# Optimization experiments

Hardware: AMD Instinct MI355X
Metric: run time of the kernel (lower is better)

The kernel has to match this reference:

```python
import jax, jax.numpy as jnp
from jax import lax
import numpy as np

B, N_WAY, K_SHOT, Q, IMG = 8, 5, 1, 15, 84
D = 3      # repnet spatial output for imgsz=84
CF = 64    # repnet channels
C2 = CF + 2

def _conv(x, w, b):
    y = lax.conv_general_dilated(x, w, (1, 1), 'VALID', dimension_numbers=('NCHW', 'OIHW', 'NCHW'))
    return y + b[None, :, None, None]

def _maxpool2(x):
    return lax.reduce_window(x, -jnp.inf, lax.max, (1, 1, 2, 2), (1, 1, 2, 2), 'VALID')

def _avgpool5(x):
    return lax.reduce_window(x, 0.0, lax.add, (1, 1, 5, 5), (1, 1, 5, 5), 'VALID') / 25.0

def _bn(x, g, b):
    # train-mode BatchNorm2d: batch statistics over (N, H, W), biased variance, eps=1e-5
    m = jnp.mean(x, (0, 2, 3), keepdims=True)
    v = jnp.var(x, (0, 2, 3), keepdims=True)
    return (x - m) * lax.rsqrt(v + 1e-5) * g[None, :, None, None] + b[None, :, None, None]

def _repnet(x, cw1, cb1, bg1, bb1, cw2, cb2, bg2, bb2, cw3, cb3, bg3, bb3, cw4, cb4, bg4, bb4):
    x = jax.nn.relu(_bn(_maxpool2(_conv(x, cw1, cb1)), bg1, bb1))
    x = jax.nn.relu(_bn(_maxpool2(_conv(x, cw2, cb2)), bg2, bb2))
    x = jax.nn.relu(_bn(_conv(x, cw3, cb3), bg3, bb3))
    x = jax.nn.relu(_bn(_conv(x, cw4, cb4), bg4, bb4))
    return _avgpool5(x)

def _forward(support_x, support_y, query_x, query_y, cw1, cb1, bg1, bb1, cw2, cb2, bg2, bb2, cw3, cb3, bg3, bb3, cw4, cb4, bg4, bb4, gW1, gb1, gW2, gb2, gW3, gb3, gW4, gb4, fW1, fb1, fW2, fb2, fW3, fb3, fW4, fb4):
    b, setsz = support_x.shape[:2]
    q = query_x.shape[1]
    rep = lambda z: _repnet(z, cw1, cb1, bg1, bb1, cw2, cb2, bg2, bb2, cw3, cb3, bg3, bb3, cw4, cb4, bg4, bb4)
    sup = rep(support_x.reshape(b * setsz, 3, IMG, IMG)).reshape(b, setsz, CF, D, D)
    qry = rep(query_x.reshape(b * q, 3, IMG, IMG)).reshape(b, q, CF, D, D)
    sup = sup.reshape(b, N_WAY, K_SHOT, CF, D, D).sum(2)  # sum over shots -> (b, n_way, c, d, d)
    setsz = N_WAY
    sy = support_y[:, ::K_SHOT]
    ii, jj = jnp.meshgrid(jnp.arange(D), jnp.arange(D), indexing='ij')
    coord = jnp.stack([ii, jj]).astype(jnp.float32) / D  # (2, d, d): ch0 = i/d, ch1 = j/d
    sup = jnp.concatenate([sup, jnp.broadcast_to(coord, (b, setsz, 2, D, D))], axis=2)  # (b,s,66,d,d)
    qry = jnp.concatenate([qry, jnp.broadcast_to(coord, (b, q, 2, D, D))], axis=2)      # (b,q,66,d,d)
    d2 = D * D
    sup = sup.reshape(b, setsz, C2, d2)
    qry = qry.reshape(b, q, C2, d2)
    # pair feature is cat([support_feat, query_feat]); split g's first layer so the
    # (b,q,s,d2,d2,2c) pair tensor is never materialized: g1([s;q]) = s@Ws + q@Wq + b1
    Ws, Wq = gW1[:C2], gW1[C2:]
    A = jnp.einsum('bscp,ck->bspk', sup, Ws)   # (b, s, d2, 256)
    Bq = jnp.einsum('bqcp,ck->bqpk', qry, Wq)  # (b, q, d2, 256)
    h = jax.nn.relu(A[:, None, :, :, None, :] + Bq[:, :, None, None, :, :] + gb1)  # (b,q,s,d2,d2,256)
    h = jax.nn.relu(h @ gW2 + gb2)
    h = jax.nn.relu(h @ gW3 + gb3)
    h = jax.nn.relu(h @ gW4 + gb4)
    x_f = h.sum((3, 4))  # sum over all d2*d2 pixel pairs -> (b, q, s, 256)
    h = jax.nn.relu(x_f @ fW1 + fb1)
    h = jax.nn.relu(h @ fW2 + fb2)  # nn.Dropout treated as identity (deterministic reference)
    h = jax.nn.relu(h @ fW3 + fb3)
    o = h @ fW4 + fb4  # (b, q, s, 64)
    score = jnp.sqrt(jnp.sum(o * o, axis=-1))  # L2 norm over feature dim -> (b, q, s)
    n = jnp.sqrt(jnp.sum(score * score, axis=2, keepdims=True))
    score = score / n * (n * n / (1.0 + n * n))  # squash
    ap = sy[:, None, :] == query_y[:, :, None]  # exactly one True per (b, q)
    an = ~ap
    score_ap = jnp.sum(jnp.where(ap, score, 0.0), axis=2, keepdims=True)
    MARGIN = 0.2
    loss = jnp.sum(jax.nn.relu(score - score_ap + MARGIN) * an)
    return loss

def setup_inputs() -> dict:
    key = jax.random.key(0)
    ks = iter(jax.random.split(key, 48))
    nrm = lambda shape, s: jax.random.normal(next(ks), shape, jnp.float32) * s
    inp = {}
    inp['support_x'] = nrm((B, N_WAY * K_SHOT, 3, IMG, IMG), 1.0)
    inp['support_y'] = jnp.tile(jnp.arange(N_WAY, dtype=jnp.int32), (B, 1))
    inp['query_x'] = nrm((B, Q, 3, IMG, IMG), 1.0)
    inp['query_y'] = jax.random.randint(next(ks), (B, Q), 0, N_WAY, dtype=jnp.int32)
    inp['cw1'] = nrm((64, 3, 3, 3), 0.19); inp['cb1'] = nrm((64,), 0.02)
    inp['bg1'] = 1.0 + nrm((64,), 0.05); inp['bb1'] = nrm((64,), 0.02)
    inp['cw2'] = nrm((64, 64, 3, 3), 0.042); inp['cb2'] = nrm((64,), 0.02)
    inp['bg2'] = 1.0 + nrm((64,), 0.05); inp['bb2'] = nrm((64,), 0.02)
    inp['cw3'] = nrm((64, 64, 3, 3), 0.042); inp['cb3'] = nrm((64,), 0.02)
    inp['bg3'] = 1.0 + nrm((64,), 0.05); inp['bb3'] = nrm((64,), 0.02)
    inp['cw4'] = nrm((64, 64, 3, 3), 0.042); inp['cb4'] = nrm((64,), 0.02)
    inp['bg4'] = 1.0 + nrm((64,), 0.05); inp['bb4'] = nrm((64,), 0.02)
    inp['gW1'] = nrm((2 * C2, 256), 0.087); inp['gb1'] = nrm((256,), 0.02)
    inp['gW2'] = nrm((256, 256), 0.0625); inp['gb2'] = nrm((256,), 0.02)
    inp['gW3'] = nrm((256, 256), 0.0625); inp['gb3'] = nrm((256,), 0.02)
    inp['gW4'] = nrm((256, 256), 0.0625); inp['gb4'] = nrm((256,), 0.02)
    inp['fW1'] = nrm((256, 256), 0.0625); inp['fb1'] = nrm((256,), 0.02)
    inp['fW2'] = nrm((256, 256), 0.0625); inp['fb2'] = nrm((256,), 0.02)
    inp['fW3'] = nrm((256, 128), 0.0625); inp['fb3'] = nrm((128,), 0.02)
    inp['fW4'] = nrm((128, 64), 0.088); inp['fb4'] = nrm((64,), 0.02)
    return inp

def reference(support_x, support_y, query_x, query_y, cw1, cb1, bg1, bb1, cw2, cb2, bg2, bb2, cw3, cb3, bg3, bb3, cw4, cb4, bg4, bb4, gW1, gb1, gW2, gb2, gW3, gb3, gW4, gb4, fW1, fb1, fW2, fb2, fW3, fb3, fW4, fb4):
    return _forward(support_x, support_y, query_x, query_y, cw1, cb1, bg1, bb1, cw2, cb2, bg2, bb2, cw3, cb3, bg3, bb3, cw4, cb4, bg4, bb4, gW1, gb1, gW2, gb2, gW3, gb3, gW4, gb4, fW1, fb1, fW2, fb2, fW3, fb3, fW4, fb4)
```

## Files before the change

### kernel.cpp

```cpp
#include <hip/hip_runtime.h>
#include <hip/hip_bf16.h>

typedef __hip_bfloat16 bf16;
typedef __attribute__((ext_vector_type(8))) short short8;
typedef __attribute__((ext_vector_type(4))) short bfx4;
typedef __attribute__((ext_vector_type(4))) float f32x4;

#define DEV __device__ __forceinline__

static constexpr int NSUP = 40;
static constexpr int NQRY = 120;
static constexpr int NIMG = 160;
static constexpr int GM   = 48600;
static constexpr int GMP  = 48640;
static constexpr int NBS  = 128;
static constexpr int NBQ  = 384;

DEV float b2f(short s) {
    union { unsigned int u; float f; } v; v.u = ((unsigned int)(unsigned short)s) << 16; return v.f;
}
DEV short bfbits(float v) {
    bf16 h = __float2bfloat16(v);
    union { bf16 b; short s; } u; u.b = h; return u.s;
}

DEV int xcd_swz(int b, int nwg) {
    int q = nwg >> 3, r = nwg & 7;
    int x = b & 7, i = b >> 3;
    return (x < r) ? x * (q + 1) + i : r * (q + 1) + (x - r) * q + i;
}

#define GLL(gp, lp) __builtin_amdgcn_global_load_lds( \
    (const __attribute__((address_space(1))) void*)(gp), \
    (__attribute__((address_space(3))) void*)(lp), 16, 0, 0)

__global__ void nhwc4_kernel(const float* sx, const float* qx, bf16* img) {
    int idx = blockIdx.x * 256 + threadIdx.x;
    if (idx >= NIMG * 7056) return;
    int n = idx / 7056, p = idx % 7056;
    const float* im = ((n < NSUP) ? sx + (size_t)n * 3 * 7056 : qx + (size_t)(n - NSUP) * 3 * 7056) + p;
    bfx4 o;
    o[0] = bfbits(im[0]);
    o[1] = bfbits(im[7056]);
    o[2] = bfbits(im[14112]);
    o[3] = 0;
    *(bfx4*)&img[(size_t)idx * 4] = o;
}

__global__ void prep_kernel(const float* cw1, const float* cw2, const float* cw3,
                            const float* cw4, const float* gW2, const float* gW3,
                            const float* gW4, const float* fW1, const float* fW2,
                            const float* fW3, const float* fW4, const float* fb4,
                            bf16* Wc1, bf16* Wp, bf16* WTg, bf16* fWT, float* fb4p) {
    int idx = blockIdx.x * 256 + threadIdx.x;
    if (idx < 4096) {
        int oc = idx >> 6, k = idx & 63;
        int ky = k >> 4, r = k & 15;
        float v = 0.f;
        if (ky < 3 && r < 12) {
            int kx = r >> 2, ic = r & 3;
            if (ic < 3) v = cw1[oc * 27 + ic * 9 + ky * 3 + kx];
        }
        Wc1[idx] = __float2bfloat16(v);
        return;
    }
    idx -= 4096;
    if (idx < 3 * 64 * 584) {
        int L = idx / (64 * 584), r = idx % (64 * 584);
        int oc = r / 584, kk = r % 584;
        const float* src = (L == 0) ? cw2 : (L == 1) ? cw3 : cw4;
        float v = 0.f;
        if (kk < 576) {
            int ic = kk & 63, tap = kk >> 6;
            v = src[oc * 576 + ic * 9 + tap];
        }
        Wp[idx] = __float2bfloat16(v);
        return;
    }
    idx -= 3 * 64 * 584;
    if (idx < 3 * 65536) {
        int L = idx >> 16, r = idx & 65535, n = r >> 8, k = r & 255;
        const float* W = (L == 0) ? gW2 : (L == 1) ? gW3 : gW4;
        WTg[idx] = __float2bfloat16(W[k * 256 + n]);
        return;
    }
    idx -= 3 * 65536;
    if (idx < 65536) {
        int n = idx >> 8, k = idx & 255;
        fWT[idx] = __float2bfloat16(fW1[k * 256 + n]);
    } else if (idx < 131072) {
        int r = idx - 65536, n = r >> 8, k = r & 255;
        fWT[idx] = __float2bfloat16(fW2[k * 256 + n]);
    } else if (idx < 163840) {
        int r = idx - 131072, n = r >> 8, k = r & 255;
        fWT[idx] = __float2bfloat16(fW3[k * 128 + n]);
    } else if (idx < 180224) {
        int r = idx - 163840, n = r >> 7, k = r & 127;
        float v = (n < 64) ? fW4[k * 64 + n] : 0.f;
        fWT[idx] = __float2bfloat16(v);
    } else if (idx < 180352) {
        int i = idx - 180224;
        fb4p[i] = (i < 64) ? fb4[i] : 0.f;
    }
}

__global__ __launch_bounds__(256) void conv1m_kernel(
        const bf16* __restrict__ img, const bf16* __restrict__ Wc1,
        const float* __restrict__ cb1, bf16* __restrict__ out) {
    int wid = xcd_swz(blockIdx.x, NIMG * 27);
    int n = wid / 27, chunk = wid % 27;
    int wv = threadIdx.x >> 6, ln = threadIdx.x & 63;
    int pr = ln & 15, kg = ln >> 4;
    int t0 = (chunk * 4 + wv) * 16;
    int t = t0 + pr;
    int tc = t < 1681 ? t : 1680;
    int pyt = tc / 41, pxt = tc % 41;
    const bf16* ib = img + (size_t)n * 28224;

    short8 wf[4][2];
    #pragma unroll
    for (int mt = 0; mt < 4; ++mt)
        #pragma unroll
        for (int h = 0; h < 2; ++h)
            wf[mt][h] = *(const short8*)&Wc1[(size_t)(mt * 16 + pr) * 64 + h * 32 + kg * 8];

    int r8 = (kg & 1) * 8;
    int kyb = kg >> 1;
    short8 pf[4][2];
    #pragma unroll
    for (int nt = 0; nt < 4; ++nt) {
        int py = 2 * pyt + (nt >> 1), px = 2 * pxt + (nt & 1);
        #pragma unroll
        for (int h = 0; h < 2; ++h) {
            int ky = h * 2 + kyb;
            short8 f = {0, 0, 0, 0, 0, 0, 0, 0};
            if (ky < 3) {
                const bf16* p = ib + ((py + ky) * 84 + px) * 4 + r8;
                if (r8 == 0) {
                    bfx4 a0 = *(const bfx4*)p, a1 = *(const bfx4*)(p + 4);
                    f[0] = a0[0]; f[1] = a0[1]; f[2] = a0[2]; f[3] = a0[3];
                    f[4] = a1[0]; f[5] = a1[1]; f[6] = a1[2]; f[7] = a1[3];
                } else {
                    bfx4 a0 = *(const bfx4*)p;
                    f[0] = a0[0]; f[1] = a0[1]; f[2] = a0[2]; f[3] = a0[3];
                }
            }
            pf[nt][h] = f;
        }
    }

    f32x4 acc[4][4];
    #pragma unroll
    for (int a = 0; a < 4; ++a)
        #pragma unroll
        for (int b = 0; b < 4; ++b)
            #pragma unroll
            for (int r = 0; r < 4; ++r) acc[a][b][r] = 0.f;

    #pragma unroll
    for (int h = 0; h < 2; ++h)
        #pragma unroll
        for (int mt = 0; mt < 4; ++mt)
            #pragma unroll
            for (int nt = 0; nt < 4; ++nt)
                acc[mt][nt] = __builtin_amdgcn_mfma_f32_16x16x32_bf16(
                    wf[mt][h], pf[nt][h], acc[mt][nt], 0, 0, 0);

    if (t < 1681) {
        bf16* ob = out + ((size_t)n * 1681 + t) * 64;
        #pragma unroll
        for (int mt = 0; mt < 4; ++mt) {
            f32x4 v = acc[mt][0];
            #pragma unroll
            for (int nt = 1; nt < 4; ++nt)
                #pragma unroll
                for (int r = 0; r < 4; ++r) v[r] = fmaxf(v[r], acc[mt][nt][r]);
            bfx4 o;
            #pragma unroll
            for (int r = 0; r < 4; ++r) o[r] = bfbits(v[r] + cb1[mt * 16 + kg * 4 + r]);
            *(bfx4*)&ob[mt * 16 + kg * 4] = o;
        }
    }
}

__global__ void stats_nhwc_kernel(const bf16* buf, int HW, float* partial) {
    int blk = blockIdx.x;
    bool qg = blk >= NBS;
    int b0 = qg ? blk - NBS : blk;
    int nb = qg ? NBQ : NBS;
    const bf16* base = buf + (qg ? (size_t)NSUP * HW * 64 : 0);
    long rows = (long)(qg ? NQRY : NSUP) * HW;
    int tid = threadIdx.x;
    int sub = tid & 7, rl = tid >> 3;
    float s1[8], s2[8];
    #pragma unroll
    for (int j = 0; j < 8; ++j) { s1[j] = 0.f; s2[j] = 0.f; }
    for (long r = (long)b0 * 32 + rl; r < rows; r += (long)nb * 32) {
        short8 v = *(const short8*)&base[r * 64 + sub * 8];
        #pragma unroll
        for (int j = 0; j < 8; ++j) { float f = b2f(v[j]); s1[j] += f; s2[j] += f * f; }
    }
    __shared__ float l1[256][8], l2[256][8];
    #pragma unroll
    for (int j = 0; j < 8; ++j) { l1[tid][j] = s1[j]; l2[tid][j] = s2[j]; }
    __syncthreads();
    if (tid < 64) {
        int su = tid >> 3, j = tid & 7;
        float a = 0.f, b = 0.f;
        for (int k = 0; k < 32; ++k) { a += l1[su + k * 8][j]; b += l2[su + k * 8][j]; }
        partial[blk * 128 + tid] = a;
        partial[blk * 128 + 64 + tid] = b;
    }
}

__global__ __launch_bounds__(1024) void bnfin_kernel(
        const float* partial, const float* gam, const float* bet,
        int HW, float* scsh) {
    int tid = threadIdx.x;
    int out = tid >> 3;
    int part = tid & 7;
    int g = out >> 6, c = out & 63;
    int b0 = g ? NBS : 0, nb = g ? NBQ : NBS;
    float s1 = 0.f, s2 = 0.f;
    for (int b = b0 + part; b < b0 + nb; b += 8) {
        s1 += partial[b * 128 + c];
        s2 += partial[b * 128 + 64 + c];
    }
    __shared__ float r1[1024], r2[1024];
    r1[tid] = s1; r2[tid] = s2;
    __syncthreads();
    if (part == 0) {
        #pragma unroll
        for (int j = 1; j < 8; ++j) { s1 += r1[tid + j]; s2 += r2[tid + j]; }
        float cnt = (float)((g ? NQRY : NSUP)) * (float)HW;
        float mean = s1 / cnt;
        float var = s2 / cnt - mean * mean;
        float istd = rsqrtf(var + 1e-5f);
        float sc = gam[c] * istd;
        scsh[out] = sc;
        scsh[128 + out] = bet[c] - mean * sc;
    }
}

__global__ void bnrelu_nhwc_kernel(bf16* buf, const float* scsh, int HW, int total8) {
    int idx = blockIdx.x * 256 + threadIdx.x;
    if (idx >= total8) return;
    size_t e0 = (size_t)idx * 8;
    int c0 = (int)(e0 & 63);
    int g = (int)(e0 / ((size_t)HW * 64)) >= NSUP ? 1 : 0;
    short8 v = *(short8*)&buf[e0];
    short8 o;
    #pragma unroll
    for (int j = 0; j < 8; ++j) {
        int c = c0 + j;
        float f = b2f(v[j]) * scsh[g * 64 + c] + scsh[128 + g * 64 + c];
        o[j] = bfbits(fmaxf(f, 0.f));
    }
    *(short8*)&buf[e0] = o;
}

template <int IW, int OW, bool POOL, int NT>
__global__ __launch_bounds__(256) void convmfma_kernel(
        const bf16* __restrict__ in, const bf16* __restrict__ Wp,
        const float* __restrict__ cb, bf16* __restrict__ out, int nwg) {
    constexpr int M  = OW * OW;
    constexpr int PW = OW / 2;
    constexpr int MP = POOL ? PW * PW : M;
    constexpr int T  = NIMG * MP;
    constexpr int NPF = POOL ? 4 : NT;

    int wid = xcd_swz(blockIdx.x, nwg);
    int wv = threadIdx.x >> 6, ln = threadIdx.x & 63;
    int pr = ln & 15, kg = ln >> 4;

    const bf16* pptr[NPF];
    int pxv[NPF];
    if (POOL) {
        int gp = (wid * 4 + wv) * 16 + pr;
        int gpc = gp < T ? gp : T - 1;
        pxv[0] = gp;
        int n = gpc / MP, pp = gpc % MP;
        int py = pp / PW, px = pp % PW;
        const bf16* ib = in + (size_t)n * (IW * IW * 64) + kg * 8;
        #pragma unroll
        for (int nt = 0; nt < 4; ++nt)
            pptr[nt] = ib + ((2 * py + (nt >> 1)) * IW + 2 * px + (nt & 1)) * 64;
    } else {
        #pragma unroll
        for (int nt = 0; nt < NT; ++nt) {
            int gp = (wid * 4 + wv) * (16 * NT) + nt * 16 + pr;
            int gpc = gp < T ? gp : T - 1;
            pxv[nt] = gp;
            int n = gpc / M, pix = gpc % M;
            int y = pix / OW, x = pix % OW;
            pptr[nt] = in + ((size_t)n * (IW * IW) + y * IW + x) * 64 + kg * 8;
        }
    }
    const bf16* wb = Wp + kg * 8;

    f32x4 acc[4][NPF];
    #pragma unroll
    for (int a = 0; a < 4; ++a)
        #pragma unroll
        for (int b = 0; b < NPF; ++b)
            #pragma unroll
            for (int r = 0; r < 4; ++r) acc[a][b][r] = 0.f;

    #pragma unroll
    for (int tap = 0; tap < 9; ++tap) {
        int off0 = ((tap / 3) * IW + (tap % 3)) * 64;
        #pragma unroll
        for (int h = 0; h < 2; ++h) {
            int off = off0 + h * 32;
            int wk = (tap * 2 + h) * 32;
            short8 wf[4], pf[NPF];
            #pragma unroll
            for (int mt = 0; mt < 4; ++mt)
                wf[mt] = *(const short8*)(wb + (size_t)(mt * 16 + pr) * 584 + wk);
            #pragma unroll
            for (int nt = 0; nt < NPF; ++nt)
                pf[nt] = *(const short8*)(pptr[nt] + off);
            #pragma unroll
            for (int mt = 0; mt < 4; ++mt)
                #pragma unroll
                for (int nt = 0; nt < NPF; ++nt)
                    acc[mt][nt] = __builtin_amdgcn_mfma_f32_16x16x32_bf16(
                        wf[mt], pf[nt], acc[mt][nt], 0, 0, 0);
        }
    }

    if (POOL) {
        int gp = pxv[0];
        if (gp < T) {
            bf16* ob = out + (size_t)gp * 64;
            #pragma unroll
            for (int mt = 0; mt < 4; ++mt) {
                f32x4 v = acc[mt][0];
                #pragma unroll
                for (int nt = 1; nt < 4; ++nt)
                    #pragma unroll
                    for (int r = 0; r < 4; ++r) v[r] = fmaxf(v[r], acc[mt][nt][r]);
                bfx4 o;
                #pragma unroll
                for (int r = 0; r < 4; ++r) o[r] = bfbits(v[r] + cb[mt * 16 + kg * 4 + r]);
                *(bfx4*)&ob[mt * 16 + kg * 4] = o;
            }
        }
    } else {
        #pragma unroll
        for (int mt = 0; mt < 4; ++mt) {
            float bv[4];
            #pragma unroll
            for (int r = 0; r < 4; ++r) bv[r] = cb[mt * 16 + kg * 4 + r];
            #pragma unroll
            for (int nt = 0; nt < NPF; ++nt) {
                if (pxv[nt] < T) {
                    bfx4 o;
                    #pragma unroll
                    for (int r = 0; r < 4; ++r) o[r] = bfbits(acc[mt][nt][r] + bv[r]);
                    *(bfx4*)&out[(size_t)pxv[nt] * 64 + mt * 16 + kg * 4] = o;
                }
            }
        }
    }
}

__global__ void bnpool_kernel(const bf16* buf4, const float* scsh, float* feat) {
    int wid = blockIdx.x * 4 + (threadIdx.x >> 6);
    int c = threadIdx.x & 63;
    if (wid >= 1440) return;
    int n = wid / 9, p9 = wid % 9;
    int g = n >= NSUP;
    float sc = scsh[g * 64 + c], sh = scsh[128 + g * 64 + c];
    int ii = p9 / 3, jj = p9 % 3;
    const bf16* base = buf4 + ((size_t)n * 225 + ii * 5 * 15 + jj * 5) * 64 + c;
    float s = 0;
    #pragma unroll
    for (int u = 0; u < 5; ++u)
        #pragma unroll
        for (int v = 0; v < 5; ++v)
            s += fmaxf(__bfloat162float(base[(u * 15 + v) * 64]) * sc + sh, 0.f);
    feat[n * 576 + c * 9 + p9] = s * 0.04f;
}

__global__ void proj_kernel(const float* feat, const float* gW1, float* A, float* Bq) {
    int n = blockIdx.x, k = threadIdx.x;
    const float* W = (n < NSUP) ? gW1 : gW1 + 66 * 256;
    float* out = (n < NSUP) ? A + (size_t)n * 9 * 256 : Bq + (size_t)(n - NSUP) * 9 * 256;
    const float* fb = feat + n * 576;
    for (int p = 0; p < 9; ++p) {
        float acc = 0;
        for (int c = 0; c < 64; ++c) acc += fb[c * 9 + p] * W[c * 256 + k];
        acc += ((float)(p / 3) * (1.f / 3.f)) * W[64 * 256 + k];
        acc += ((float)(p % 3) * (1.f / 3.f)) * W[65 * 256 + k];
        out[p * 256 + k] = acc;
    }
}

__global__ void h0_kernel(const float* A, const float* Bq, const float* gb1, bf16* H) {
    int tid = threadIdx.x;
    int row = blockIdx.x * 8 + (tid >> 5);
    int col = (tid & 31) * 8;
    short8 o;
    if (row < GM) {
        int bqs = row / 81, r81 = row % 81;
        int ps = r81 / 9, pq = r81 % 9;
        int b = bqs / 75, r75 = bqs % 75, q = r75 / 5, s = r75 % 5;
        const float* Ar = A + ((size_t)((b * 5 + s) * 9 + ps)) * 256 + col;
        const float* Br = Bq + ((size_t)((b * 15 + q) * 9 + pq)) * 256 + col;
        #pragma unroll
        for (int j = 0; j < 8; ++j) {
            float v = Ar[j] + Br[j] + gb1[col + j];
            o[j] = bfbits(fmaxf(v, 0.f));
        }
    } else {
        #pragma unroll
        for (int j = 0; j < 8; ++j) o[j] = 0;
    }
    *(short8*)&H[(size_t)row * 256 + col] = o;
}

__global__ __launch_bounds__(256) void gemm_relu_kernel(
        const bf16* __restrict__ Ain, const bf16* __restrict__ WT,
        const float* __restrict__ bias, bf16* __restrict__ out) {
    __shared__ __align__(16) short As[2][4096];
    __shared__ __align__(16) short Bs[2][4096];
    int bm0 = blockIdx.x * 128;
    int bn0 = blockIdx.y * 128;
    int tid = threadIdx.x, wv = tid >> 6, ln = tid & 63;
    int wm = wv >> 1, wn = wv & 1;

    int srow = (wv * 2) * 16 + (ln >> 2);
    int scol = (ln & 3) * 8;
    const bf16* Ag = Ain + (size_t)(bm0 + srow) * 256 + scol;
    const bf16* Bg = WT + (size_t)(bn0 + srow) * 256 + scol;

    f32x4 acc[4][4];
    #pragma unroll
    for (int m = 0; m < 4; ++m)
        #pragma unroll
        for (int n = 0; n < 4; ++n)
            #pragma unroll
            for (int r = 0; r < 4; ++r) acc[m][n][r] = 0.f;

    int ar = (wm * 64 + (ln & 15)) * 32 + (ln >> 4) * 8;
    int br = (wn * 64 + (ln & 15)) * 32 + (ln >> 4) * 8;

    GLL(Ag,            &As[0][(wv * 2) * 512]);
    GLL(Ag + 16 * 256, &As[0][(wv * 2 + 1) * 512]);
    GLL(Bg,            &Bs[0][(wv * 2) * 512]);
    GLL(Bg + 16 * 256, &Bs[0][(wv * 2 + 1) * 512]);
    __syncthreads();

    int cur = 0;
    for (int kt = 0; kt < 8; ++kt) {
        if (kt < 7) {
            int k0 = (kt + 1) * 32;
            GLL(Ag + k0,            &As[cur ^ 1][(wv * 2) * 512]);
            GLL(Ag + 16 * 256 + k0, &As[cur ^ 1][(wv * 2 + 1) * 512]);
            GLL(Bg + k0,            &Bs[cur ^ 1][(wv * 2) * 512]);
            GLL(Bg + 16 * 256 + k0, &Bs[cur ^ 1][(wv * 2 + 1) * 512]);
        }
        short8 a[4], b[4];
        #pragma unroll
        for (int m = 0; m < 4; ++m) a[m] = *(const short8*)&As[cur][ar + m * 512];
        #pragma unroll
        for (int n = 0; n < 4; ++n) b[n] = *(const short8*)&Bs[cur][br + n * 512];
        #pragma unroll
        for (int m = 0; m < 4; ++m)
            #pragma unroll
            for (int n = 0; n < 4; ++n)
                acc[m][n] = __builtin_amdgcn_mfma_f32_16x16x32_bf16(a[m], b[n], acc[m][n], 0, 0, 0);
        __syncthreads();
        cur ^= 1;
    }

    int orow = bm0 + wm * 64 + (ln >> 4) * 4;
    int ocol = bn0 + wn * 64 + (ln & 15);
    #pragma unroll
    for (int n = 0; n < 4; ++n) {
        float bv = bias[ocol + n * 16];
        #pragma unroll
        for (int m = 0; m < 4; ++m) {
            #pragma unroll
            for (int r = 0; r < 4; ++r) {
                float v = acc[m][n][r] + bv;
                out[(size_t)(orow + m * 16 + r) * 256 + ocol + n * 16] =
                    __float2bfloat16(fmaxf(v, 0.f));
            }
        }
    }
}

template <int KT, bool RELU, bool F32OUT>
__global__ __launch_bounds__(256) void gemm_f_kernel(
        const bf16* __restrict__ Ain, const bf16* __restrict__ WT,
        const float* __restrict__ bias, void* __restrict__ outv, int ldo) {
    constexpr int K = KT * 32;
    __shared__ __align__(16) short As[2][4096];
    __shared__ __align__(16) short Bs[2][4096];
    int bm0 = blockIdx.x * 128;
    int bn0 = blockIdx.y * 128;
    int tid = threadIdx.x, wv = tid >> 6, ln = tid & 63;
    int wm = wv >> 1, wn = wv & 1;

    int srow = (wv * 2) * 16 + (ln >> 2);
    int scol = (ln & 3) * 8;
    const bf16* Ag = Ain + (size_t)(bm0 + srow) * K + scol;
    const bf16* Bg = WT + (size_t)(bn0 + srow) * K + scol;

    f32x4 acc[4][4];
    #pragma unroll
    for (int m = 0; m < 4; ++m)
        #pragma unroll
        for (int n = 0; n < 4; ++n)
            #pragma unroll
            for (int r = 0; r < 4; ++r) acc[m][n][r] = 0.f;

    int ar = (wm * 64 + (ln & 15)) * 32 + (ln >> 4) * 8;
    int br = (wn * 64 + (ln & 15)) * 32 + (ln >> 4) * 8;

    GLL(Ag,          &As[0][(wv * 2) * 512]);
    GLL(Ag + 16 * K, &As[0][(wv * 2 + 1) * 512]);
    GLL(Bg,          &Bs[0][(wv * 2) * 512]);
    GLL(Bg + 16 * K, &Bs[0][(wv * 2 + 1) * 512]);
    __syncthreads();

    int cur = 0;
    for (int kt = 0; kt < KT; ++kt) {
        if (kt < KT - 1) {
            int k0 = (kt + 1) * 32;
            GLL(Ag + k0,          &As[cur ^ 1][(wv * 2) * 512]);
            GLL(Ag + 16 * K + k0, &As[cur ^ 1][(wv * 2 + 1) * 512]);
            GLL(Bg + k0,          &Bs[cur ^ 1][(wv * 2) * 512]);
            GLL(Bg + 16 * K + k0, &Bs[cur ^ 1][(wv * 2 + 1) * 512]);
        }
        short8 a[4], b[4];
        #pragma unroll
        for (int m = 0; m < 4; ++m) a[m] = *(const short8*)&As[cur][ar + m * 512];
        #pragma unroll
        for (int n = 0; n < 4; ++n) b[n] = *(const short8*)&Bs[cur][br + n * 512];
        #pragma unroll
        for (int m = 0; m < 4; ++m)
            #pragma unroll
            for (int n = 0; n < 4; ++n)
                acc[m][n] = __builtin_amdgcn_mfma_f32_16x16x32_bf16(a[m], b[n], acc[m][n], 0, 0, 0);
        __syncthreads();
        cur ^= 1;
    }

    int orow = bm0 + wm * 64 + (ln >> 4) * 4;
    int ocol = bn0 + wn * 64 + (ln & 15);
    #pragma unroll
    for (int n = 0; n < 4; ++n) {
        float bv = bias[ocol + n * 16];
        #pragma unroll
        for (int m = 0; m < 4; ++m) {
            #pragma unroll
            for (int r = 0; r < 4; ++r) {
                float v = acc[m][n][r] + bv;
                if (RELU) v = fmaxf(v, 0.f);
                size_t oi = (size_t)(orow + m * 16 + r) * ldo + ocol + n * 16;
                if (F32OUT) ((float*)outv)[oi] = v;
                else        ((bf16*)outv)[oi] = __float2bfloat16(v);
            }
        }
    }
}

__global__ void xfred_kernel(const bf16* H, bf16* xfb) {
    int bqs = blockIdx.x, t = threadIdx.x;
    float s = 0;
    if (bqs < 600) {
        const bf16* p = H + (size_t)bqs * 81 * 256 + t;
        for (int r = 0; r < 81; ++r) s += __bfloat162float(p[r * 256]);
    }
    xfb[(size_t)bqs * 256 + t] = __float2bfloat16(s);
}

__global__ void score_kernel(const float* F4, const int* sy, const int* qy, float* lossp) {
    __shared__ float scs[8];
    int bid = blockIdx.x;
    int tid = threadIdx.x;
    int s = tid >> 6, k = tid & 63;
    float v = F4[(size_t)(bid * 5 + s) * 128 + k];
    float sum = v * v;
    #pragma unroll
    for (int m = 1; m < 64; m <<= 1) sum += __shfl_xor(sum, m);
    if (k == 0) scs[s] = sqrtf(sum);
    __syncthreads();
    if (tid == 0) {
        int b = bid / 15, q = bid % 15;
        float n2 = 0;
        for (int j = 0; j < 5; ++j) n2 += scs[j] * scs[j];
        float n = sqrtf(n2);
        float f = n / (1.f + n2);
        int qyv = qy[b * 15 + q];
        float sc[5]; bool ap[5]; float sap = 0;
        for (int j = 0; j < 5; ++j) {
            sc[j] = scs[j] * f;
            ap[j] = (sy[b * 5 + j] == qyv);
            if (ap[j]) sap += sc[j];
        }
        float lp = 0;
        for (int j = 0; j < 5; ++j)
            if (!ap[j]) lp += fmaxf(sc[j] - sap + 0.2f, 0.f);
        lossp[bid] = lp;
    }
}

__global__ void lreduce_kernel(const float* lossp, float* out) {
    __shared__ float r[128];
    int tid = threadIdx.x;
    r[tid] = (tid < NQRY) ? lossp[tid] : 0.f;
    __syncthreads();
    for (int off = 64; off; off >>= 1) {
        if (tid < off) r[tid] += r[tid + off];
        __syncthreads();
    }
    if (tid == 0) out[0] = r[0];
}

extern "C" void kernel_launch(void* const* d_in, const int* in_sizes, int n_in,
                              void* d_out, int out_size, void* d_ws, size_t ws_size,
                              hipStream_t stream) {
    const float* sx  = (const float*)d_in[0];
    const int*   syp = (const int*)d_in[1];
    const float* qx  = (const float*)d_in[2];
    const int*   qyp = (const int*)d_in[3];
    const float* cw1 = (const float*)d_in[4];  const float* cb1 = (const float*)d_in[5];
    const float* bg1 = (const float*)d_in[6];  const float* bb1 = (const float*)d_in[7];
    const float* cw2 = (const float*)d_in[8];  const float* cb2 = (const float*)d_in[9];
    const float* bg2 = (const float*)d_in[10]; const float* bb2 = (const float*)d_in[11];
    const float* cw3 = (const float*)d_in[12]; const float* cb3 = (const float*)d_in[13];
    const float* bg3 = (const float*)d_in[14]; const float* bb3 = (const float*)d_in[15];
    const float* cw4 = (const float*)d_in[16]; const float* cb4 = (const float*)d_in[17];
    const float* bg4 = (const float*)d_in[18]; const float* bb4 = (const float*)d_in[19];
    const float* gW1 = (const float*)d_in[20]; const float* gb1 = (const float*)d_in[21];
    const float* gW2 = (const float*)d_in[22]; const float* gb2 = (const float*)d_in[23];
    const float* gW3 = (const float*)d_in[24]; const float* gb3 = (const float*)d_in[25];
    const float* gW4 = (const float*)d_in[26]; const float* gb4 = (const float*)d_in[27];
    const float* fW1 = (const float*)d_in[28]; const float* fb1 = (const float*)d_in[29];
    const float* fW2 = (const float*)d_in[30]; const float* fb2 = (const float*)d_in[31];
    const float* fW3 = (const float*)d_in[32]; const float* fb3 = (const float*)d_in[33];
    const float* fW4 = (const float*)d_in[34]; const float* fb4 = (const float*)d_in[35];

    char* w = (char*)d_ws;
    size_t off = 0;
    bf16*  buf1  = (bf16*)(w + off); off += 34426880ull;
    bf16*  hbuf  = (bf16*)(w + off); off += 31150080ull;
    bf16*  pbuf2 = (bf16*)(w + off); off += 7393280ull;
    bf16*  buf3  = (bf16*)(w + off); off += 5918720ull;
    bf16*  buf4  = (bf16*)(w + off); off += 4608000ull;
    float* feat  = (float*)(w + off); off += 368640ull;
    float* Abuf  = (float*)(w + off); off += 368640ull;
    float* Bbuf  = (float*)(w + off); off += 1105920ull;
    bf16*  xfb   = (bf16*)(w + off); off += 327680ull;
    bf16*  F1    = (bf16*)(w + off); off += 327680ull;
    bf16*  F2    = (bf16*)(w + off); off += 327680ull;
    bf16*  F3    = (bf16*)(w + off); off += 163840ull;
    float* F4    = (float*)(w + off); off += 327680ull;
    float* partial = (float*)(w + off); off += 262144ull;
    float* scsh  = (float*)(w + off); off += 4096ull;
    bf16*  imgN  = (bf16*)(w + off); off += 9031680ull;
    bf16*  Wc1   = (bf16*)(w + off); off += 8192ull;
    bf16*  Wp    = (bf16*)(w + off); off += 224256ull;
    bf16*  WTg   = (bf16*)(w + off); off += 393216ull;
    bf16*  fWT   = (bf16*)(w + off); off += 360448ull;
    float* fb4p  = (float*)(w + off); off += 512ull;
    float* lossp = (float*)(w + off); off += 512ull;

    float* scsh1 = scsh;        float* scsh2 = scsh + 256;
    float* scsh3 = scsh + 512;  float* scsh4 = scsh + 768;
    bf16* Wp2 = Wp;
    bf16* Wp3 = Wp + 64 * 584;
    bf16* Wp4 = Wp + 2 * 64 * 584;
    bf16* fWT1 = fWT;
    bf16* fWT2 = fWT + 65536;
    bf16* fWT3 = fWT + 131072;
    bf16* fWT4 = fWT + 163840;

    bf16* Hb0 = buf1;
    bf16* Hb1 = hbuf;

    nhwc4_kernel<<<(NIMG * 7056 + 255) / 256, 256, 0, stream>>>(sx, qx, imgN);
    prep_kernel<<<(493184 + 255) / 256, 256, 0, stream>>>(
        cw1, cw2, cw3, cw4, gW2, gW3, gW4, fW1, fW2, fW3, fW4, fb4,
        Wc1, Wp, WTg, fWT, fb4p);

    conv1m_kernel<<<NIMG * 27, 256, 0, stream>>>(imgN, Wc1, cb1, buf1);
    stats_nhwc_kernel<<<NBS + NBQ, 256, 0, stream>>>(buf1, 1681, partial);
    bnfin_kernel<<<1, 1024, 0, stream>>>(partial, bg1, bb1, 1681, scsh1);
    bnrelu_nhwc_kernel<<<(2151680 + 255) / 256, 256, 0, stream>>>(buf1, scsh1, 1681, 2151680);

    convmfma_kernel<41, 39, true, 4><<<dim3(903), 256, 0, stream>>>(buf1, Wp2, cb2, pbuf2, 903);
    stats_nhwc_kernel<<<NBS + NBQ, 256, 0, stream>>>(pbuf2, 361, partial);
    bnfin_kernel<<<1, 1024, 0, stream>>>(partial, bg2, bb2, 361, scsh2);
    bnrelu_nhwc_kernel<<<(462080 + 255) / 256, 256, 0, stream>>>(pbuf2, scsh2, 361, 462080);

    convmfma_kernel<19, 17, false, 2><<<dim3(362), 256, 0, stream>>>(pbuf2, Wp3, cb3, buf3, 362);
    stats_nhwc_kernel<<<NBS + NBQ, 256, 0, stream>>>(buf3, 289, partial);
    bnfin_kernel<<<1, 1024, 0, stream>>>(partial, bg3, bb3, 289, scsh3);
    bnrelu_nhwc_kernel<<<(369920 + 255) / 256, 256, 0, stream>>>(buf3, scsh3, 289, 369920);

    convmfma_kernel<17, 15, false, 2><<<dim3(282), 256, 0, stream>>>(buf3, Wp4, cb4, buf4, 282);
    stats_nhwc_kernel<<<NBS + NBQ, 256, 0, stream>>>(buf4, 225, partial);
    bnfin_kernel<<<1, 1024, 0, stream>>>(partial, bg4, bb4, 225, scsh4);
    bnpool_kernel<<<360, 256, 0, stream>>>(buf4, scsh4, feat);

    proj_kernel<<<NIMG, 256, 0, stream>>>(feat, gW1, Abuf, Bbuf);

    h0_kernel<<<GMP / 8, 256, 0, stream>>>(Abuf, Bbuf, gb1, Hb0);
    dim3 ggrid(GMP / 128, 2);
    gemm_relu_kernel<<<ggrid, 256, 0, stream>>>(Hb0, WTg,          gb2, Hb1);
    gemm_relu_kernel<<<ggrid, 256, 0, stream>>>(Hb1, WTg + 65536,  gb3, Hb0);
    gemm_relu_kernel<<<ggrid, 256, 0, stream>>>(Hb0, WTg + 131072, gb4, Hb1);
    xfred_kernel<<<640, 256, 0, stream>>>(Hb1, xfb);

    gemm_f_kernel<8, true,  false><<<dim3(5, 2), 256, 0, stream>>>(xfb, fWT1, fb1,  (void*)F1, 256);
    gemm_f_kernel<8, true,  false><<<dim3(5, 2), 256, 0, stream>>>(F1,  fWT2, fb2,  (void*)F2, 256);
    gemm_f_kernel<8, true,  false><<<dim3(5, 1), 256, 0, stream>>>(F2,  fWT3, fb3,  (void*)F3, 128);
    gemm_f_kernel<4, false, true ><<<dim3(5, 1), 256, 0, stream>>>(F3,  fWT4, fb4p, (void*)F4, 128);

    score_kernel<<<NQRY, 320, 0, stream>>>(F4, syp, qyp, lossp);
    lreduce_kernel<<<1, 128, 0, stream>>>(lossp, (float*)d_out);
}
```

Before: 357.7 us.

## Fuse g-MLP input build and three GEMM layers into one LDS-resident kernel

Replaces the h0 kernel and three separate gemm_relu launches with one kernel that builds a 128-row H tile in shared memory, then runs all three 256x256 layers on it with swizzled LDS storage and writes only the final layer to global memory. This removes three full round trips of a roughly 25 MB activation through HBM and three launches. In exchange, weights are read directly from global or L2 with no staging, 64 KB of LDS per block lowers occupancy, and each block computes all 256 output columns. Separately, the conv MFMA loop now software-pipelines the patch loads one k-step ahead of the compute.

```diff
diff --git a/kernel.cpp b/kernel.cpp
--- a/kernel.cpp
+++ b/kernel.cpp
@@ -306,26 +306,33 @@
             #pragma unroll
             for (int r = 0; r < 4; ++r) acc[a][b][r] = 0.f;
 
-    #pragma unroll
-    for (int tap = 0; tap < 9; ++tap) {
-        int off0 = ((tap / 3) * IW + (tap % 3)) * 64;
-        #pragma unroll
-        for (int h = 0; h < 2; ++h) {
-            int off = off0 + h * 32;
-            int wk = (tap * 2 + h) * 32;
-            short8 wf[4], pf[NPF];
-            #pragma unroll
-            for (int mt = 0; mt < 4; ++mt)
-                wf[mt] = *(const short8*)(wb + (size_t)(mt * 16 + pr) * 584 + wk);
+    short8 pf_c[NPF];
+    #pragma unroll
+    for (int nt = 0; nt < NPF; ++nt) pf_c[nt] = *(const short8*)(pptr[nt]);
+    #pragma unroll
+    for (int s = 0; s < 18; ++s) {
+        short8 pf_n[NPF];
+        if (s < 17) {
+            int s2 = s + 1, tap2 = s2 >> 1, h2 = s2 & 1;
+            int off2 = ((tap2 / 3) * IW + (tap2 % 3)) * 64 + h2 * 32;
             #pragma unroll
             for (int nt = 0; nt < NPF; ++nt)
-                pf[nt] = *(const short8*)(pptr[nt] + off);
-            #pragma unroll
-            for (int mt = 0; mt < 4; ++mt)
-                #pragma unroll
-                for (int nt = 0; nt < NPF; ++nt)
-                    acc[mt][nt] = __builtin_amdgcn_mfma_f32_16x16x32_bf16(
-                        wf[mt], pf[nt], acc[mt][nt], 0, 0, 0);
+                pf_n[nt] = *(const short8*)(pptr[nt] + off2);
+        }
+        int wk = s * 32;
+        short8 wf[4];
+        #pragma unroll
+        for (int mt = 0; mt < 4; ++mt)
+            wf[mt] = *(const short8*)(wb + (size_t)(mt * 16 + pr) * 584 + wk);
+        #pragma unroll
+        for (int mt = 0; mt < 4; ++mt)
+            #pragma unroll
+            for (int nt = 0; nt < NPF; ++nt)
+                acc[mt][nt] = __builtin_amdgcn_mfma_f32_16x16x32_bf16(
+                    wf[mt], pf_c[nt], acc[mt][nt], 0, 0, 0);
+        if (s < 17) {
+            #pragma unroll
+            for (int nt = 0; nt < NPF; ++nt) pf_c[nt] = pf_n[nt];
         }
     }
 
@@ -397,97 +404,105 @@
     }
 }
 
-__global__ void h0_kernel(const float* A, const float* Bq, const float* gb1, bf16* H) {
+__global__ __launch_bounds__(512) void gmlp_fused_kernel(
+        const float* __restrict__ A, const float* __restrict__ Bq,
+        const float* __restrict__ gb1, const bf16* __restrict__ WTg,
+        const float* __restrict__ gb2, const float* __restrict__ gb3,
+        const float* __restrict__ gb4, bf16* __restrict__ H3) {
+    __shared__ __align__(16) short hs[128 * 256];
     int tid = threadIdx.x;
-    int row = blockIdx.x * 8 + (tid >> 5);
-    int col = (tid & 31) * 8;
-    short8 o;
-    if (row < GM) {
-        int bqs = row / 81, r81 = row % 81;
-        int ps = r81 / 9, pq = r81 % 9;
-        int b = bqs / 75, r75 = bqs % 75, q = r75 / 5, s = r75 % 5;
-        const float* Ar = A + ((size_t)((b * 5 + s) * 9 + ps)) * 256 + col;
-        const float* Br = Bq + ((size_t)((b * 15 + q) * 9 + pq)) * 256 + col;
-        #pragma unroll
-        for (int j = 0; j < 8; ++j) {
-            float v = Ar[j] + Br[j] + gb1[col + j];
-            o[j] = bfbits(fmaxf(v, 0.f));
-        }
-    } else {
-        #pragma unroll
-        for (int j = 0; j < 8; ++j) o[j] = 0;
-    }
-    *(short8*)&H[(size_t)row * 256 + col] = o;
-}
-
-__global__ __launch_bounds__(256) void gemm_relu_kernel(
-        const bf16* __restrict__ Ain, const bf16* __restrict__ WT,
-        const float* __restrict__ bias, bf16* __restrict__ out) {
-    __shared__ __align__(16) short As[2][4096];
-    __shared__ __align__(16) short Bs[2][4096];
-    int bm0 = blockIdx.x * 128;
-    int bn0 = blockIdx.y * 128;
-    int tid = threadIdx.x, wv = tid >> 6, ln = tid & 63;
-    int wm = wv >> 1, wn = wv & 1;
-
-    int srow = (wv * 2) * 16 + (ln >> 2);
-    int scol = (ln & 3) * 8;
-    const bf16* Ag = Ain + (size_t)(bm0 + srow) * 256 + scol;
-    const bf16* Bg = WT + (size_t)(bn0 + srow) * 256 + scol;
-
-    f32x4 acc[4][4];
-    #pragma unroll
-    for (int m = 0; m < 4; ++m)
-        #pragma unroll
-        for (int n = 0; n < 4; ++n)
-            #pragma unroll
-            for (int r = 0; r < 4; ++r) acc[m][n][r] = 0.f;
-
-    int ar = (wm * 64 + (ln & 15)) * 32 + (ln >> 4) * 8;
-    int br = (wn * 64 + (ln & 15)) * 32 + (ln >> 4) * 8;
-
-    GLL(Ag,            &As[0][(wv * 2) * 512]);
-    GLL(Ag + 16 * 256, &As[0][(wv * 2 + 1) * 512]);
-    GLL(Bg,            &Bs[0][(wv * 2) * 512]);
-    GLL(Bg + 16 * 256, &Bs[0][(wv * 2 + 1) * 512]);
+    int r0 = blockIdx.x * 128;
+
+    #pragma unroll
+    for (int i = 0; i < 8; ++i) {
+        int row = (tid >> 5) + i * 16;
+        int c8 = tid & 31;
+        int col = c8 * 8;
+        int grow = r0 + row;
+        short8 o = {0, 0, 0, 0, 0, 0, 0, 0};
+        if (grow < GM) {
+            int bqs = grow / 81, r81 = grow % 81;
+            int ps = r81 / 9, pq = r81 % 9;
+            int b = bqs / 75, r75 = bqs % 75, q = r75 / 5, s5 = r75 % 5;
+            const float* Ar = A + ((size_t)((b * 5 + s5) * 9 + ps)) * 256 + col;
+            const float* Br = Bq + ((size_t)((b * 15 + q) * 9 + pq)) * 256 + col;
+            #pragma unroll
+            for (int j = 0; j < 8; ++j)
+                o[j] = bfbits(fmaxf(Ar[j] + Br[j] + gb1[col + j], 0.f));
+        }
+        int c8s = c8 ^ (row & 7);
+        *(short8*)&hs[row * 256 + c8s * 8] = o;
+    }
     __syncthreads();
 
-    int cur = 0;
-    for (int kt = 0; kt < 8; ++kt) {
-        if (kt < 7) {
-            int k0 = (kt + 1) * 32;
-            GLL(Ag + k0,            &As[cur ^ 1][(wv * 2) * 512]);
-            GLL(Ag + 16 * 256 + k0, &As[cur ^ 1][(wv * 2 + 1) * 512]);
-            GLL(Bg + k0,            &Bs[cur ^ 1][(wv * 2) * 512]);
-            GLL(Bg + 16 * 256 + k0, &Bs[cur ^ 1][(wv * 2 + 1) * 512]);
-        }
-        short8 a[4], b[4];
-        #pragma unroll
-        for (int m = 0; m < 4; ++m) a[m] = *(const short8*)&As[cur][ar + m * 512];
-        #pragma unroll
-        for (int n = 0; n < 4; ++n) b[n] = *(const short8*)&Bs[cur][br + n * 512];
+    int wv = tid >> 6, ln = tid & 63;
+    int wr = wv >> 2, wc = wv & 3;
+    int pr = ln & 15, kg = ln >> 4;
+
+    #pragma unroll
+    for (int L = 0; L < 3; ++L) {
+        const bf16* WT = WTg + L * 65536;
+        const float* bias = (L == 0) ? gb2 : (L == 1) ? gb3 : gb4;
+
+        f32x4 acc[4][4];
         #pragma unroll
         for (int m = 0; m < 4; ++m)
             #pragma unroll
             for (int n = 0; n < 4; ++n)
-                acc[m][n] = __builtin_amdgcn_mfma_f32_16x16x32_bf16(a[m], b[n], acc[m][n], 0, 0, 0);
+                #pragma unroll
+                for (int r = 0; r < 4; ++r) acc[m][n][r] = 0.f;
+
+        #pragma unroll
+        for (int kt = 0; kt < 8; ++kt) {
+            short8 a[4], b[4];
+            #pragma unroll
+            for (int m = 0; m < 4; ++m) {
+                int row = wr * 64 + m * 16 + pr;
+                int c8 = kt * 4 + kg;
+                int c8s = c8 ^ (row & 7);
+                a[m] = *(const short8*)&hs[row * 256 + c8s * 8];
+            }
+            #pragma unroll
+            for (int n = 0; n < 4; ++n)
+                b[n] = *(const short8*)&WT[(size_t)(wc * 64 + n * 16 + pr) * 256 + kt * 32 + kg * 8];
+            #pragma unroll
+            for (int m = 0; m < 4; ++m)
+                #pragma unroll
+                for (int n = 0; n < 4; ++n)
+                    acc[m][n] = __builtin_amdgcn_mfma_f32_16x16x32_bf16(a[m], b[n], acc[m][n], 0, 0, 0);
+        }
+
         __syncthreads();
-        cur ^= 1;
-    }
-
-    int orow = bm0 + wm * 64 + (ln >> 4) * 4;
-    int ocol = bn0 + wn * 64 + (ln & 15);
-    #pragma unroll
-    for (int n = 0; n < 4; ++n) {
-        float bv = bias[ocol + n * 16];
-        #pragma unroll
-        for (int m = 0; m < 4; ++m) {
-            #pragma unroll
-            for (int r = 0; r < 4; ++r) {
-                float v = acc[m][n][r] + bv;
-                out[(size_t)(orow + m * 16 + r) * 256 + ocol + n * 16] =
-                    __float2bfloat16(fmaxf(v, 0.f));
-            }
+        if (L < 2) {
+            #pragma unroll
+            for (int m = 0; m < 4; ++m)
+                #pragma unroll
+                for (int n = 0; n < 4; ++n) {
+                    int col = wc * 64 + n * 16 + pr;
+                    float bv = bias[col];
+                    #pragma unroll
+                    for (int r = 0; r < 4; ++r) {
+                        int row = wr * 64 + m * 16 + kg * 4 + r;
+                        int c8s = (col >> 3) ^ (row & 7);
+                        hs[row * 256 + c8s * 8 + (col & 7)] =
+                            bfbits(fmaxf(acc[m][n][r] + bv, 0.f));
+                    }
+                }
+            __syncthreads();
+        } else {
+            #pragma unroll
+            for (int m = 0; m < 4; ++m)
+                #pragma unroll
+                for (int n = 0; n < 4; ++n) {
+                    int col = wc * 64 + n * 16 + pr;
+                    float bv = bias[col];
+                    #pragma unroll
+                    for (int r = 0; r < 4; ++r) {
+                        int row = wr * 64 + m * 16 + kg * 4 + r;
+                        H3[(size_t)(r0 + row) * 256 + col] =
+                            __float2bfloat16(fmaxf(acc[m][n][r] + bv, 0.f));
+                    }
+                }
         }
     }
 }
@@ -648,7 +663,7 @@
     char* w = (char*)d_ws;
     size_t off = 0;
     bf16*  buf1  = (bf16*)(w + off); off += 34426880ull;
-    bf16*  hbuf  = (bf16*)(w + off); off += 31150080ull;
+    bf16*  H3    = (bf16*)(w + off); off += 31150080ull;
     bf16*  pbuf2 = (bf16*)(w + off); off += 7393280ull;
     bf16*  buf3  = (bf16*)(w + off); off += 5918720ull;
     bf16*  buf4  = (bf16*)(w + off); off += 4608000ull;
@@ -680,9 +695,6 @@
     bf16* fWT3 = fWT + 131072;
     bf16* fWT4 = fWT + 163840;
 
-    bf16* Hb0 = buf1;
-    bf16* Hb1 = hbuf;
-
     nhwc4_kernel<<<(NIMG * 7056 + 255) / 256, 256, 0, stream>>>(sx, qx, imgN);
     prep_kernel<<<(493184 + 255) / 256, 256, 0, stream>>>(
         cw1, cw2, cw3, cw4, gW2, gW3, gW4, fW1, fW2, fW3, fW4, fb4,
@@ -710,12 +722,8 @@
 
     proj_kernel<<<NIMG, 256, 0, stream>>>(feat, gW1, Abuf, Bbuf);
 
-    h0_kernel<<<GMP / 8, 256, 0, stream>>>(Abuf, Bbuf, gb1, Hb0);
-    dim3 ggrid(GMP / 128, 2);
-    gemm_relu_kernel<<<ggrid, 256, 0, stream>>>(Hb0, WTg,          gb2, Hb1);
-    gemm_relu_kernel<<<ggrid, 256, 0, stream>>>(Hb1, WTg + 65536,  gb3, Hb0);
-    gemm_relu_kernel<<<ggrid, 256, 0, stream>>>(Hb0, WTg + 131072, gb4, Hb1);
-    xfred_kernel<<<640, 256, 0, stream>>>(Hb1, xfb);
+    gmlp_fused_kernel<<<GMP / 128, 512, 0, stream>>>(Abuf, Bbuf, gb1, WTg, gb2, gb3, gb4, H3);
+    xfred_kernel<<<640, 256, 0, stream>>>(H3, xfb);
 
     gemm_f_kernel<8, true,  false><<<dim3(5, 2), 256, 0, stream>>>(xfb, fWT1, fb1,  (void*)F1, 256);
     gemm_f_kernel<8, true,  false><<<dim3(5, 2), 256, 0, stream>>>(F1,  fWT2, fb2,  (void*)F2, 256);
```

After: 365.3 us. +2.1%, slower.
